# Kernel optimization log

Hardware: AMD Instinct MI355X
Metric: run time of the kernel (lower is better)

Reference implementation:

```python
import jax, jax.numpy as jnp
import numpy as np

P = 16       # patch size
HEADS = 4    # attention heads
ROPE_BASE = 10000.0


def _ln(x, g, b, eps=1e-5):
    m = x.mean(-1, keepdims=True)
    v = jnp.var(x, axis=-1, keepdims=True)
    return (x - m) / jnp.sqrt(v + eps) * g + b


def _rope(x, cos, sin):
    # x: (B, N, D); cos/sin: (N, D//2); rotate consecutive pairs
    B, N, D = x.shape
    x2 = x.reshape(B, N, D // 2, 2)
    x0, x1 = x2[..., 0], x2[..., 1]
    r0 = x0 * cos - x1 * sin
    r1 = x0 * sin + x1 * cos
    return jnp.stack([r0, r1], axis=-1).reshape(B, N, D)


def setup_inputs() -> dict:
    key = jax.random.key(0)
    L, D, Hd, Cin, S, NC = 8, 256, 1024, 3, 512, 1000
    ks = jax.random.split(key, 16)
    nrm = lambda k, shape, s=0.02: jax.random.normal(k, shape, jnp.float32) * s
    f32 = jnp.float32
    return {
        "x": jax.random.normal(ks[0], (16, Cin, S, S), f32),
        "conv_w": nrm(ks[1], (D, Cin, P, P)),
        "conv_b": jnp.zeros((D,), f32),
        "cls_tok": nrm(ks[2], (1, 1, D)),
        "ln1_g": jnp.ones((L, D), f32), "ln1_b": jnp.zeros((L, D), f32),
        "wq": nrm(ks[3], (L, D, D)), "bq": jnp.zeros((L, D), f32),
        "wk": nrm(ks[4], (L, D, D)), "bk": jnp.zeros((L, D), f32),
        "wv": nrm(ks[5], (L, D, D)), "bv": jnp.zeros((L, D), f32),
        "wo": nrm(ks[6], (L, D, D)), "bo": jnp.zeros((L, D), f32),
        "ln2_g": jnp.ones((L, D), f32), "ln2_b": jnp.zeros((L, D), f32),
        "w1": nrm(ks[7], (L, D, Hd)), "b1": jnp.zeros((L, Hd), f32),
        "w2": nrm(ks[8], (L, Hd, D)), "b2": jnp.zeros((L, D), f32),
        "lnf_g": jnp.ones((D,), f32), "lnf_b": jnp.zeros((D,), f32),
        "head_w": nrm(ks[9], (D, NC)), "head_b": jnp.zeros((NC,), f32),
    }


def reference(x, conv_w, conv_b, cls_tok, ln1_g, ln1_b, wq, bq, wk, bk, wv, bv,
              wo, bo, ln2_g, ln2_b, w1, b1, w2, b2, lnf_g, lnf_b, head_w, head_b):
    B, C, H, W = x.shape
    D = conv_w.shape[0]
    dh = D // HEADS
    # patch embed: conv with stride==kernel == blocked einsum
    xp = x.reshape(B, C, H // P, P, W // P, P)
    patches = jnp.einsum('bchpwq,dcpq->bhwd', xp, conv_w).reshape(B, -1, D) + conv_b
    tok = jnp.concatenate([jnp.broadcast_to(cls_tok, (B, 1, D)), patches], axis=1)
    N = tok.shape[1]  # n_patches + 1
    # rope tables over full d_model (applied pre head-split, as pos_module(q,k,pos))
    pos = jnp.arange(N, dtype=jnp.float32)
    inv_freq = 1.0 / (ROPE_BASE ** (jnp.arange(0, D, 2, dtype=jnp.float32) / D))
    ang = pos[:, None] * inv_freq                    # (N, D/2)
    cos, sin = jnp.cos(ang), jnp.sin(ang)
    scale = 1.0 / np.sqrt(dh).astype(np.float32)

    def block(h, p):
        l1g, l1b, Wq, Bq, Wk, Bk, Wv, Bv, Wo, Bo, l2g, l2b, W1, B1, W2, B2 = p
        y = _ln(h, l1g, l1b)
        q = _rope(y @ Wq + Bq, cos, sin)
        k = _rope(y @ Wk + Bk, cos, sin)
        v = y @ Wv + Bv
        qh = q.reshape(B, N, HEADS, dh)
        kh = k.reshape(B, N, HEADS, dh)
        vh = v.reshape(B, N, HEADS, dh)
        sc = jnp.einsum('bqhd,bkhd->bhqk', qh, kh) * scale
        a = jax.nn.softmax(sc, axis=-1)
        ctx = jnp.einsum('bhqk,bkhd->bqhd', a, vh).reshape(B, N, D)
        h = h + (ctx @ Wo + Bo)
        y2 = _ln(h, l2g, l2b)
        h = h + jax.nn.gelu(y2 @ W1 + B1, approximate=False) @ W2 + B2
        return h, None

    params = (ln1_g, ln1_b, wq, bq, wk, bk, wv, bv, wo, bo, ln2_g, ln2_b, w1, b1, w2, b2)
    out, _ = jax.lax.scan(block, tok, params)
    out = _ln(out, lnf_g, lnf_b)
    return out[:, 0] @ head_w + head_b
```

## Files before the change

### kernel.cpp

```cpp
#include <hip/hip_runtime.h>
#include <hip/hip_bf16.h>
#include <math.h>

#define BATCH 16
#define CIN 3
#define SIMG 512
#define PPATCH 16
#define DMODEL 256
#define HIDDEN 1024
#define LAYERS 8
#define NHEADS 4
#define DHEAD 64
#define NTOK 1025
#define NROWS (BATCH * NTOK)
#define NCLS 1000
#define VSTR 1032

typedef __attribute__((ext_vector_type(8))) short bf16x8;
typedef __attribute__((ext_vector_type(4))) float f32x4;

#define MFMA16(a, b, c) __builtin_amdgcn_mfma_f32_16x16x32_bf16(a, b, c, 0, 0, 0)

__device__ __forceinline__ ushort f2bf(float f) {
    union { float f; unsigned u; } v; v.f = f;
    unsigned r = v.u + 0x7fff + ((v.u >> 16) & 1);
    return (ushort)(r >> 16);
}
__device__ __forceinline__ float bf2f(ushort u) {
    union { unsigned u; float f; } v; v.u = ((unsigned)u) << 16;
    return v.f;
}
__device__ __forceinline__ unsigned pk2(ushort a, ushort b) {
    return (unsigned)a | ((unsigned)b << 16);
}
__device__ __forceinline__ int swz16(int row, int bcol) {
    return row * 128 + (bcol ^ ((row & 7) << 4));
}
__device__ __forceinline__ void gload16(const void* g, void* l) {
    __builtin_amdgcn_global_load_lds(
        (const __attribute__((address_space(1))) unsigned int*)g,
        (__attribute__((address_space(3))) unsigned int*)l,
        16, 0, 0);
}

__global__ void rope_tab_kernel(float* __restrict__ cosb, float* __restrict__ sinb) {
    int i = blockIdx.x * 256 + threadIdx.x;
    if (i >= NTOK * 128) return;
    int n = i >> 7, j = i & 127;
    float inv = powf(10000.0f, -(float)(2 * j) / 256.0f);
    float ang = (float)n * inv;
    cosb[i] = cosf(ang);
    sinb[i] = sinf(ang);
}

__global__ void cls_kernel(const float* __restrict__ cls, float* __restrict__ tok) {
    int i = blockIdx.x * 256 + threadIdx.x;
    int b = i >> 8, d = i & 255;
    tok[(size_t)b * NTOK * DMODEL + d] = cls[d];
}

__global__ void cvt_bf16_kernel(const float* __restrict__ in, ushort* __restrict__ out, int n) {
    int base = (blockIdx.x * 256 + threadIdx.x) * 4;
    if (base >= n) return;
    float4 v = *(const float4*)(in + base);
    *(ushort4*)(out + base) = make_ushort4(f2bf(v.x), f2bf(v.y), f2bf(v.z), f2bf(v.w));
}

__global__ __launch_bounds__(256) void transpose_cvt_kernel(
    const float* __restrict__ W, ushort* __restrict__ WT, int K, int N,
    long wl, long wtl)
{
    __shared__ float t[32][33];
    int l = blockIdx.z;
    W  += (size_t)l * wl;
    WT += (size_t)l * wtl;
    int kb = blockIdx.y * 32, nb = blockIdx.x * 32;
    int tx = threadIdx.x & 31, ty = threadIdx.x >> 5;
    #pragma unroll
    for (int i = 0; i < 32; i += 8)
        t[ty + i][tx] = W[(size_t)(kb + ty + i) * N + nb + tx];
    __syncthreads();
    #pragma unroll
    for (int i = 0; i < 32; i += 8)
        WT[(size_t)(nb + ty + i) * K + kb + tx] = f2bf(t[tx][ty + i]);
}

__global__ __launch_bounds__(256) void ln_kernel(
    const float* __restrict__ in, ushort* __restrict__ outp,
    const float* __restrict__ g, const float* __restrict__ bta, int nrows)
{
    int row = blockIdx.x * 4 + (threadIdx.x >> 6);
    int lane = threadIdx.x & 63;
    if (row >= nrows) return;
    const float* xr = in + (size_t)row * DMODEL;
    float4 v = *(const float4*)(xr + lane * 4);
    float s = v.x + v.y + v.z + v.w;
    float ss = v.x * v.x + v.y * v.y + v.z * v.z + v.w * v.w;
    #pragma unroll
    for (int m = 1; m < 64; m <<= 1) {
        s += __shfl_xor(s, m, 64);
        ss += __shfl_xor(ss, m, 64);
    }
    float mean = s * (1.0f / 256.0f);
    float var = ss * (1.0f / 256.0f) - mean * mean;
    float inv = rsqrtf(var + 1e-5f);
    float4 gv = *(const float4*)(g + lane * 4);
    float4 bv = *(const float4*)(bta + lane * 4);
    ushort4 o = make_ushort4(f2bf((v.x - mean) * inv * gv.x + bv.x),
                             f2bf((v.y - mean) * inv * gv.y + bv.y),
                             f2bf((v.z - mean) * inv * gv.z + bv.z),
                             f2bf((v.w - mean) * inv * gv.w + bv.w));
    *(ushort4*)(outp + (size_t)row * DMODEL + lane * 4) = o;
}

__global__ __launch_bounds__(256) void patch_gemm(
    const float* __restrict__ x, const ushort* __restrict__ Wb,
    const float* __restrict__ bias, float* __restrict__ h)
{
    __shared__ __align__(16) ushort As[128 * 64];
    __shared__ __align__(16) ushort Bs[64 * 64];
    int bid = blockIdx.x;
    int xcd = bid & 7, idx = bid >> 3;
    int m0 = (xcd * 16 + (idx >> 2)) * 128;
    int n0 = (idx & 3) * 64;
    int tid = threadIdx.x;
    int w = tid >> 6, l = tid & 63;
    int lr = l & 15, lg = l >> 4;
    int wm = w & 1, wn = w >> 1;
    f32x4 acc[4][2] = {};

    for (int k0 = 0; k0 < 768; k0 += 64) {
        __syncthreads();
        #pragma unroll
        for (int i = 0; i < 4; ++i) {
            int id = tid + 256 * i; int r = id >> 3, c8 = id & 7;
            int m = m0 + r;
            int b_ = m >> 10, pi = m & 1023, ph = pi >> 5, pw = pi & 31;
            int k = k0 + c8 * 8;
            int c = k >> 8, rem = k & 255, pr = rem >> 4, q = rem & 15;
            const float* src = x + ((size_t)((b_ * 3 + c) * SIMG) + ph * 16 + pr) * SIMG
                                 + pw * 16 + q;
            float4 v0 = *(const float4*)src;
            float4 v1 = *(const float4*)(src + 4);
            uint4 t;
            t.x = pk2(f2bf(v0.x), f2bf(v0.y));
            t.y = pk2(f2bf(v0.z), f2bf(v0.w));
            t.z = pk2(f2bf(v1.x), f2bf(v1.y));
            t.w = pk2(f2bf(v1.z), f2bf(v1.w));
            *(uint4*)((char*)As + swz16(r, c8 * 16)) = t;
        }
        #pragma unroll
        for (int i = 0; i < 2; ++i) {
            int id = tid + 256 * i; int r = id >> 3, c8 = id & 7;
            uint4 t = *(const uint4*)(Wb + (size_t)(n0 + r) * 768 + k0 + c8 * 8);
            *(uint4*)((char*)Bs + swz16(r, c8 * 16)) = t;
        }
        __syncthreads();
        #pragma unroll
        for (int ks = 0; ks < 2; ++ks) {
            bf16x8 af[4];
            #pragma unroll
            for (int mf = 0; mf < 4; ++mf)
                af[mf] = *(const bf16x8*)((char*)As + swz16(wm * 64 + mf * 16 + lr, ks * 64 + lg * 16));
            #pragma unroll
            for (int nf = 0; nf < 2; ++nf) {
                bf16x8 bfr = *(const bf16x8*)((char*)Bs + swz16(wn * 32 + nf * 16 + lr, ks * 64 + lg * 16));
                #pragma unroll
                for (int mf = 0; mf < 4; ++mf)
                    acc[mf][nf] = MFMA16(af[mf], bfr, acc[mf][nf]);
            }
        }
    }
    #pragma unroll
    for (int mf = 0; mf < 4; ++mf) {
        #pragma unroll
        for (int nf = 0; nf < 2; ++nf) {
            int n = n0 + wn * 32 + nf * 16 + lr;
            float bb = bias[n];
            #pragma unroll
            for (int e = 0; e < 4; ++e) {
                int m = m0 + wm * 64 + mf * 16 + lg * 4 + e;
                int b_ = m >> 10, pi = m & 1023;
                h[((size_t)(b_ * NTOK + 1 + pi)) * DMODEL + n] = acc[mf][nf][e] + bb;
            }
        }
    }
}

__global__ __launch_bounds__(512) void gemm_qkv(
    const ushort* __restrict__ A, const ushort* __restrict__ WT,
    const float* __restrict__ bq, const float* __restrict__ bk,
    const float* __restrict__ bv,
    ushort* __restrict__ qbf, ushort* __restrict__ kbf, ushort* __restrict__ vT,
    const float* __restrict__ cosb, const float* __restrict__ sinb, int M)
{
    __shared__ __align__(16) ushort As[128 * 64];
    __shared__ __align__(16) ushort Bs[128 * 64];
    int bid = blockIdx.x;
    int xcd = bid & 7, idx = bid >> 3;
    int mt = xcd * 17 + idx / 6;
    int m0 = mt * 128;
    if (m0 >= M) return;
    int n0 = (idx % 6) * 128;
    int tid = threadIdx.x;
    int w = tid >> 6, l = tid & 63;
    int lr = l & 15, lg = l >> 4;
    int wm = w & 1, wn = w >> 1;
    int wb0 = (tid & ~63) * 16;
    f32x4 acc[4][2] = {};

    for (int k0 = 0; k0 < 256; k0 += 64) {
        __syncthreads();
        #pragma unroll
        for (int i = 0; i < 2; ++i) {
            int id = tid + 512 * i; int r = id >> 3, c8 = id & 7;
            int mrow = m0 + r; if (mrow > M - 1) mrow = M - 1;
            int c8s = c8 ^ (r & 7);
            gload16(A + (size_t)mrow * 256 + k0 + c8s * 8, (char*)As + wb0 + i * 8192);
        }
        #pragma unroll
        for (int i = 0; i < 2; ++i) {
            int id = tid + 512 * i; int r = id >> 3, c8 = id & 7;
            int c8s = c8 ^ (r & 7);
            gload16(WT + (size_t)(n0 + r) * 256 + k0 + c8s * 8, (char*)Bs + wb0 + i * 8192);
        }
        __syncthreads();
        #pragma unroll
        for (int ks = 0; ks < 2; ++ks) {
            bf16x8 af[4], bf[2];
            #pragma unroll
            for (int mf = 0; mf < 4; ++mf)
                af[mf] = *(const bf16x8*)((char*)As + swz16(wm * 64 + mf * 16 + lr, ks * 64 + lg * 16));
            #pragma unroll
            for (int nf = 0; nf < 2; ++nf)
                bf[nf] = *(const bf16x8*)((char*)Bs + swz16(wn * 32 + nf * 16 + lr, ks * 64 + lg * 16));
            #pragma unroll
            for (int nf = 0; nf < 2; ++nf)
                #pragma unroll
                for (int mf = 0; mf < 4; ++mf)
                    acc[mf][nf] = MFMA16(af[mf], bf[nf], acc[mf][nf]);
        }
    }

    int sel = (n0 + wn * 32) >> 8;
    int ncb = (n0 + wn * 32) & 255;
    const float* bp = sel == 0 ? bq : (sel == 1 ? bk : bv);
    #pragma unroll
    for (int mf = 0; mf < 4; ++mf) {
        #pragma unroll
        for (int nf = 0; nf < 2; ++nf) {
            int nc = ncb + nf * 16 + lr;
            float bb = bp[nc];
            #pragma unroll
            for (int e = 0; e < 4; ++e) {
                int m = m0 + wm * 64 + mf * 16 + lg * 4 + e;
                float v = acc[mf][nf][e] + bb;
                if (sel < 2) {
                    float pv = __shfl_xor(v, 1, 64);
                    int tok = m % NTOK;
                    int j = nc >> 1;
                    float c = cosb[tok * 128 + j], s = sinb[tok * 128 + j];
                    float o = (nc & 1) ? (pv * s + v * c) : (v * c - pv * s);
                    if (m < M) {
                        ushort* dst = sel == 0 ? qbf : kbf;
                        dst[(size_t)m * DMODEL + nc] = f2bf(o);
                    }
                } else if (m < M) {
                    int b_ = m / NTOK, tok = m - b_ * NTOK;
                    vT[((size_t)(b_ * 256 + nc)) * VSTR + tok] = f2bf(v);
                }
            }
        }
    }
}

__global__ __launch_bounds__(512) void gemm_gelu(
    const ushort* __restrict__ A, const ushort* __restrict__ WT,
    const float* __restrict__ bias, ushort* __restrict__ Cbf, int M)
{
    __shared__ __align__(16) ushort As[128 * 64];
    __shared__ __align__(16) ushort Bs[128 * 64];
    int bid = blockIdx.x;
    int xcd = bid & 7, idx = bid >> 3;
    int mt = xcd * 17 + (idx >> 3);
    int m0 = mt * 128;
    if (m0 >= M) return;
    int n0 = (idx & 7) * 128;
    int tid = threadIdx.x;
    int w = tid >> 6, l = tid & 63;
    int lr = l & 15, lg = l >> 4;
    int wm = w & 1, wn = w >> 1;
    int wb0 = (tid & ~63) * 16;
    f32x4 acc[4][2] = {};

    for (int k0 = 0; k0 < 256; k0 += 64) {
        __syncthreads();
        #pragma unroll
        for (int i = 0; i < 2; ++i) {
            int id = tid + 512 * i; int r = id >> 3, c8 = id & 7;
            int mrow = m0 + r; if (mrow > M - 1) mrow = M - 1;
            int c8s = c8 ^ (r & 7);
            gload16(A + (size_t)mrow * 256 + k0 + c8s * 8, (char*)As + wb0 + i * 8192);
        }
        #pragma unroll
        for (int i = 0; i < 2; ++i) {
            int id = tid + 512 * i; int r = id >> 3, c8 = id & 7;
            int c8s = c8 ^ (r & 7);
            gload16(WT + (size_t)(n0 + r) * 256 + k0 + c8s * 8, (char*)Bs + wb0 + i * 8192);
        }
        __syncthreads();
        #pragma unroll
        for (int ks = 0; ks < 2; ++ks) {
            bf16x8 af[4], bf[2];
            #pragma unroll
            for (int mf = 0; mf < 4; ++mf)
                af[mf] = *(const bf16x8*)((char*)As + swz16(wm * 64 + mf * 16 + lr, ks * 64 + lg * 16));
            #pragma unroll
            for (int nf = 0; nf < 2; ++nf)
                bf[nf] = *(const bf16x8*)((char*)Bs + swz16(wn * 32 + nf * 16 + lr, ks * 64 + lg * 16));
            #pragma unroll
            for (int nf = 0; nf < 2; ++nf)
                #pragma unroll
                for (int mf = 0; mf < 4; ++mf)
                    acc[mf][nf] = MFMA16(af[mf], bf[nf], acc[mf][nf]);
        }
    }

    #pragma unroll
    for (int mf = 0; mf < 4; ++mf) {
        #pragma unroll
        for (int nf = 0; nf < 2; ++nf) {
            int n = n0 + wn * 32 + nf * 16 + lr;
            float bb = bias[n];
            #pragma unroll
            for (int e = 0; e < 4; ++e) {
                int m = m0 + wm * 64 + mf * 16 + lg * 4 + e;
                float v = acc[mf][nf][e] + bb;
                if (m < M) {
                    float gg = 0.5f * v * (1.0f + erff(v * 0.70710678118f));
                    Cbf[(size_t)m * HIDDEN + n] = f2bf(gg);
                }
            }
        }
    }
}

__global__ __launch_bounds__(512) void gemm_res_ln(
    const ushort* __restrict__ A, const ushort* __restrict__ WT,
    const float* __restrict__ bias, float* __restrict__ hres,
    ushort* __restrict__ ybf, const float* __restrict__ g,
    const float* __restrict__ beta, int M, int K)
{
    __shared__ __align__(16) ushort As[64 * 64];
    __shared__ __align__(16) ushort Bs[256 * 64];
    __shared__ float psum[8][64], psq[8][64];
    __shared__ float mv[64][2];
    int tid = threadIdx.x;
    int w = tid >> 6, l = tid & 63;
    int lr = l & 15, lg = l >> 4;
    int m0 = blockIdx.x * 64;
    int wb0 = (tid & ~63) * 16;
    f32x4 acc[4][2] = {};

    for (int k0 = 0; k0 < K; k0 += 64) {
        __syncthreads();
        {
            int r = tid >> 3, c8 = tid & 7;
            int mrow = m0 + r; if (mrow > M - 1) mrow = M - 1;
            int c8s = c8 ^ (r & 7);
            gload16(A + (size_t)mrow * K + k0 + c8s * 8, (char*)As + wb0);
        }
        #pragma unroll
        for (int i = 0; i < 4; ++i) {
            int id = tid + 512 * i; int r = id >> 3, c8 = id & 7;
            int c8s = c8 ^ (r & 7);
            gload16(WT + (size_t)r * K + k0 + c8s * 8, (char*)Bs + wb0 + i * 8192);
        }
        __syncthreads();
        #pragma unroll
        for (int ks = 0; ks < 2; ++ks) {
            bf16x8 af[4], bf[2];
            #pragma unroll
            for (int mf = 0; mf < 4; ++mf)
                af[mf] = *(const bf16x8*)((char*)As + swz16(mf * 16 + lr, ks * 64 + lg * 16));
            #pragma unroll
            for (int nf = 0; nf < 2; ++nf)
                bf[nf] = *(const bf16x8*)((char*)Bs + swz16(w * 32 + nf * 16 + lr, ks * 64 + lg * 16));
            #pragma unroll
            for (int nf = 0; nf < 2; ++nf)
                #pragma unroll
                for (int mf = 0; mf < 4; ++mf)
                    acc[mf][nf] = MFMA16(af[mf], bf[nf], acc[mf][nf]);
        }
    }

    #pragma unroll
    for (int mf = 0; mf < 4; ++mf) {
        #pragma unroll
        for (int nf = 0; nf < 2; ++nf) {
            int n = w * 32 + nf * 16 + lr;
            float bb = bias[n];
            #pragma unroll
            for (int e = 0; e < 4; ++e) {
                int m = m0 + mf * 16 + lg * 4 + e;
                float hv = acc[mf][nf][e] + bb;
                if (m < M) hv += hres[(size_t)m * DMODEL + n];
                acc[mf][nf][e] = hv;
            }
        }
    }
    #pragma unroll
    for (int mf = 0; mf < 4; ++mf) {
        #pragma unroll
        for (int e = 0; e < 4; ++e) {
            float s = acc[mf][0][e] + acc[mf][1][e];
            float q = acc[mf][0][e] * acc[mf][0][e] + acc[mf][1][e] * acc[mf][1][e];
            #pragma unroll
            for (int t = 1; t < 16; t <<= 1) {
                s += __shfl_xor(s, t, 16);
                q += __shfl_xor(q, t, 16);
            }
            if (lr == 0) {
                int r64 = mf * 16 + lg * 4 + e;
                psum[w][r64] = s;
                psq[w][r64] = q;
            }
        }
    }
    __syncthreads();
    if (tid < 64) {
        float s = 0.f, q = 0.f;
        #pragma unroll
        for (int ww = 0; ww < 8; ++ww) { s += psum[ww][tid]; q += psq[ww][tid]; }
        float mean = s * (1.0f / 256.0f);
        float var = q * (1.0f / 256.0f) - mean * mean;
        mv[tid][0] = mean;
        mv[tid][1] = rsqrtf(var + 1e-5f);
    }
    __syncthreads();
    #pragma unroll
    for (int mf = 0; mf < 4; ++mf) {
        #pragma unroll
        for (int e = 0; e < 4; ++e) {
            int r64 = mf * 16 + lg * 4 + e;
            int m = m0 + r64;
            if (m >= M) continue;
            float mean = mv[r64][0], rstd = mv[r64][1];
            #pragma unroll
            for (int nf = 0; nf < 2; ++nf) {
                int n = w * 32 + nf * 16 + lr;
                float hv = acc[mf][nf][e];
                hres[(size_t)m * DMODEL + n] = hv;
                ybf[(size_t)m * DMODEL + n] = f2bf((hv - mean) * rstd * g[n] + beta[n]);
            }
        }
    }
}

__global__ __launch_bounds__(256) void flash_mfma(
    const ushort* __restrict__ Qb, const ushort* __restrict__ Kb,
    const ushort* __restrict__ Vt, ushort* __restrict__ Ctx)
{
    __shared__ __align__(16) ushort QPs[64 * 64];
    __shared__ __align__(16) ushort Ks[64 * 64];
    __shared__ __align__(16) ushort Vs[64 * 64];

    int bid = blockIdx.x;
    int xcd = bid & 7, idx = bid >> 3;
    int bh = xcd * 8 + idx / 17;
    int q0 = (idx % 17) * 64;
    int tid = threadIdx.x;
    int w = tid >> 6, l = tid & 63;
    int lr = l & 15, lg = l >> 4;
    int b = bh >> 2, h = bh & 3;
    const size_t rowbase = (size_t)b * NTOK;
    const size_t vbase = (size_t)(b * 256 + h * 64) * VSTR;
    int wb0 = (tid & ~63) * 16;

    int id0 = tid, id1 = tid + 256;
    int r0 = id0 >> 3, c80 = id0 & 7;
    int r1 = id1 >> 3, c81 = id1 & 7;
    int d0 = swz16(r0, c80 * 16), d1 = swz16(r1, c81 * 16);

    {
        int qr0 = q0 + r0; if (qr0 > 1024) qr0 = 1024;
        int qr1 = q0 + r1; if (qr1 > 1024) qr1 = 1024;
        int c80s = c80 ^ (r0 & 7), c81s = c81 ^ (r1 & 7);
        gload16(Qb + (rowbase + qr0) * 256 + h * 64 + c80s * 8, (char*)QPs + wb0);
        gload16(Qb + (rowbase + qr1) * 256 + h * 64 + c81s * 8, (char*)QPs + wb0 + 4096);
    }

    uint4 kreg0, kreg1, vreg0, vreg1;
    auto loadKV = [&](int kt) {
        int kr0 = kt * 64 + r0; if (kr0 > 1024) kr0 = 1024;
        int kr1 = kt * 64 + r1; if (kr1 > 1024) kr1 = 1024;
        kreg0 = *(const uint4*)(Kb + (rowbase + kr0) * 256 + h * 64 + c80 * 8);
        kreg1 = *(const uint4*)(Kb + (rowbase + kr1) * 256 + h * 64 + c81 * 8);
        vreg0 = *(const uint4*)(Vt + vbase + (size_t)r0 * VSTR + kt * 64 + c80 * 8);
        vreg1 = *(const uint4*)(Vt + vbase + (size_t)r1 * VSTR + kt * 64 + c81 * 8);
    };
    auto writeKV = [&]() {
        *(uint4*)((char*)Ks + d0) = kreg0;
        *(uint4*)((char*)Ks + d1) = kreg1;
        *(uint4*)((char*)Vs + d0) = vreg0;
        *(uint4*)((char*)Vs + d1) = vreg1;
    };

    loadKV(0);
    __syncthreads();
    writeKV();
    __syncthreads();

    bf16x8 qreg[2];
    #pragma unroll
    for (int ks = 0; ks < 2; ++ks)
        qreg[ks] = *(const bf16x8*)((char*)QPs + swz16(w * 16 + lr, ks * 64 + lg * 16));

    f32x4 po[4] = {};
    float lsum = 0.f;

    for (int kt = 0; kt < 17; ++kt) {
        if (kt < 16) loadKV(kt + 1);

        f32x4 sa[4] = {};
        #pragma unroll
        for (int ks = 0; ks < 2; ++ks) {
            #pragma unroll
            for (int nf = 0; nf < 4; ++nf) {
                bf16x8 kb = *(const bf16x8*)((char*)Ks + swz16(nf * 16 + lr, ks * 64 + lg * 16));
                sa[nf] = MFMA16(kb, qreg[ks], sa[nf]);
            }
        }

        #pragma unroll
        for (int nf = 0; nf < 4; ++nf) {
            float p0, p1, p2, p3;
            {
                int kc0 = kt * 64 + nf * 16 + lg * 4;
                p0 = (kc0 + 0 > 1024) ? 0.f : __expf(sa[nf][0] * 0.125f);
                p1 = (kc0 + 1 > 1024) ? 0.f : __expf(sa[nf][1] * 0.125f);
                p2 = (kc0 + 2 > 1024) ? 0.f : __expf(sa[nf][2] * 0.125f);
                p3 = (kc0 + 3 > 1024) ? 0.f : __expf(sa[nf][3] * 0.125f);
            }
            lsum += (p0 + p1) + (p2 + p3);
            uint2 t;
            t.x = pk2(f2bf(p0), f2bf(p1));
            t.y = pk2(f2bf(p2), f2bf(p3));
            *(uint2*)((char*)QPs + swz16(w * 16 + lr, nf * 32 + lg * 8)) = t;
        }

        #pragma unroll
        for (int ks = 0; ks < 2; ++ks) {
            bf16x8 pa = *(const bf16x8*)((char*)QPs + swz16(w * 16 + lr, ks * 64 + lg * 16));
            #pragma unroll
            for (int d = 0; d < 4; ++d) {
                bf16x8 vb = *(const bf16x8*)((char*)Vs + swz16(d * 16 + lr, ks * 64 + lg * 16));
                po[d] = MFMA16(pa, vb, po[d]);
            }
        }

        __syncthreads();
        if (kt < 16) writeKV();
        __syncthreads();
    }

    lsum += __shfl_xor(lsum, 16, 64);
    lsum += __shfl_xor(lsum, 32, 64);
    #pragma unroll
    for (int e = 0; e < 4; ++e) {
        float le = __shfl(lsum, lg * 4 + e, 16);
        int qr = q0 + w * 16 + lg * 4 + e;
        if (qr <= 1024) {
            float inv = 1.0f / le;
            #pragma unroll
            for (int d = 0; d < 4; ++d)
                Ctx[(rowbase + qr) * 256 + h * 64 + d * 16 + lr] = f2bf(po[d][e] * inv);
        }
    }
}

__global__ void head_kernel(const ushort* __restrict__ ybf,
                            const float* __restrict__ hw,
                            const float* __restrict__ hb,
                            float* __restrict__ out)
{
    int i = blockIdx.x * 256 + threadIdx.x;
    if (i >= BATCH * NCLS) return;
    int b = i / NCLS, c = i % NCLS;
    const ushort* xr = ybf + (size_t)b * NTOK * DMODEL;
    float acc = hb[c];
    for (int t = 0; t < DMODEL; ++t) acc += bf2f(xr[t]) * hw[t * NCLS + c];
    out[i] = acc;
}

extern "C" void kernel_launch(void* const* d_in, const int* in_sizes, int n_in,
                              void* d_out, int out_size, void* d_ws, size_t ws_size,
                              hipStream_t stream) {
    const float* x      = (const float*)d_in[0];
    const float* conv_w = (const float*)d_in[1];
    const float* conv_b = (const float*)d_in[2];
    const float* cls_tok= (const float*)d_in[3];
    const float* ln1_g  = (const float*)d_in[4];
    const float* ln1_b  = (const float*)d_in[5];
    const float* wq     = (const float*)d_in[6];
    const float* bq     = (const float*)d_in[7];
    const float* wk     = (const float*)d_in[8];
    const float* bk     = (const float*)d_in[9];
    const float* wv     = (const float*)d_in[10];
    const float* bv     = (const float*)d_in[11];
    const float* wo     = (const float*)d_in[12];
    const float* bo     = (const float*)d_in[13];
    const float* ln2_g  = (const float*)d_in[14];
    const float* ln2_b  = (const float*)d_in[15];
    const float* w1     = (const float*)d_in[16];
    const float* b1     = (const float*)d_in[17];
    const float* w2     = (const float*)d_in[18];
    const float* b2     = (const float*)d_in[19];
    const float* lnf_g  = (const float*)d_in[20];
    const float* lnf_b  = (const float*)d_in[21];
    const float* head_w = (const float*)d_in[22];
    const float* head_b = (const float*)d_in[23];

    char* p = (char*)d_ws;
    float* h    = (float*)p;            p += (size_t)NROWS * DMODEL * 4;
    float* cosb = (float*)p;            p += (size_t)NTOK * 128 * 4;
    float* sinb = (float*)p;            p += (size_t)NTOK * 128 * 4;
    ushort* ybf = (ushort*)p;           p += (size_t)NROWS * DMODEL * 2;
    ushort* cbf = (ushort*)p;           p += (size_t)NROWS * DMODEL * 2;
    ushort* qbf = (ushort*)p;           p += (size_t)NROWS * DMODEL * 2;
    ushort* kbf = (ushort*)p;           p += (size_t)NROWS * DMODEL * 2;
    ushort* vT  = (ushort*)p;           p += (size_t)BATCH * 256 * VSTR * 2 + 256;
    ushort* hidbf = (ushort*)p;         p += (size_t)NROWS * HIDDEN * 2;
    ushort* wqkvT = (ushort*)p;         p += (size_t)LAYERS * 768 * DMODEL * 2;
    ushort* woT = (ushort*)p;           p += (size_t)LAYERS * DMODEL * DMODEL * 2;
    ushort* w1T = (ushort*)p;           p += (size_t)LAYERS * DMODEL * HIDDEN * 2;
    ushort* w2T = (ushort*)p;           p += (size_t)LAYERS * DMODEL * HIDDEN * 2;
    ushort* cwb = (ushort*)p;           p += (size_t)DMODEL * 768 * 2;

    transpose_cvt_kernel<<<dim3(8, 8, LAYERS), 256, 0, stream>>>(
        wq, wqkvT, 256, 256, 65536, 196608);
    transpose_cvt_kernel<<<dim3(8, 8, LAYERS), 256, 0, stream>>>(
        wk, wqkvT + 65536, 256, 256, 65536, 196608);
    transpose_cvt_kernel<<<dim3(8, 8, LAYERS), 256, 0, stream>>>(
        wv, wqkvT + 131072, 256, 256, 65536, 196608);
    transpose_cvt_kernel<<<dim3(8, 8, LAYERS), 256, 0, stream>>>(
        wo, woT, 256, 256, 65536, 65536);
    transpose_cvt_kernel<<<dim3(32, 8, LAYERS), 256, 0, stream>>>(
        w1, w1T, 256, 1024, 262144, 262144);
    transpose_cvt_kernel<<<dim3(8, 32, LAYERS), 256, 0, stream>>>(
        w2, w2T, 1024, 256, 262144, 262144);
    rope_tab_kernel<<<(NTOK * 128 + 255) / 256, 256, 0, stream>>>(cosb, sinb);
    cls_kernel<<<BATCH, 256, 0, stream>>>(cls_tok, h);
    cvt_bf16_kernel<<<192, 256, 0, stream>>>(conv_w, cwb, DMODEL * 768);
    patch_gemm<<<512, 256, 0, stream>>>(x, cwb, conv_b, h);

    const int M = NROWS;
    int grln = (M + 63) / 64;

    ln_kernel<<<(M + 3) / 4, 256, 0, stream>>>(h, ybf, ln1_g, ln1_b, M);

    for (int l = 0; l < LAYERS; ++l) {
        const ushort* WqkvT = wqkvT + (size_t)l * 768 * DMODEL;
        const ushort* WoT = woT + (size_t)l * DMODEL * DMODEL;
        const ushort* W1T = w1T + (size_t)l * DMODEL * HIDDEN;
        const ushort* W2T = w2T + (size_t)l * DMODEL * HIDDEN;

        gemm_qkv<<<816, 512, 0, stream>>>(ybf, WqkvT, bq + l * DMODEL, bk + l * DMODEL,
                                          bv + l * DMODEL, qbf, kbf, vT, cosb, sinb, M);
        flash_mfma<<<1088, 256, 0, stream>>>(qbf, kbf, vT, cbf);
        gemm_res_ln<<<grln, 512, 0, stream>>>(cbf, WoT, bo + l * DMODEL, h, ybf,
                                              ln2_g + l * DMODEL, ln2_b + l * DMODEL,
                                              M, DMODEL);
        gemm_gelu<<<1088, 512, 0, stream>>>(ybf, W1T, b1 + l * HIDDEN, hidbf, M);
        const float* ng = (l < LAYERS - 1) ? ln1_g + (l + 1) * DMODEL : lnf_g;
        const float* nb = (l < LAYERS - 1) ? ln1_b + (l + 1) * DMODEL : lnf_b;
        gemm_res_ln<<<grln, 512, 0, stream>>>(hidbf, W2T, b2 + l * DMODEL, h, ybf,
                                              ng, nb, M, HIDDEN);
    }
    head_kernel<<<(BATCH * NCLS + 255) / 256, 256, 0, stream>>>(ybf, head_w, head_b,
                                                                (float*)d_out);
}
```

Baseline: 1.234 ms.

## Process two 64-row query subtiles per flash-attention block to reuse K/V tiles

Each attention block now covers 128 queries as two 64-row subtiles. Both subtiles share each staged K/V tile, which halves K/V global loads per query and halves the grid size. Q fragments are loaded straight from global memory into registers instead of going through shared memory, and one startup barrier is dropped. In exchange, the last query tile (a single valid row) now wastes a full 128-row tile of compute, register use per thread rises, and the smaller grid may balance less well across CUs.

Result: slower. 1.309 ms (+6.0%).

```diff
diff --git a/kernel.cpp b/kernel.cpp
--- a/kernel.cpp
+++ b/kernel.cpp
@@ -461,33 +461,33 @@
     const ushort* __restrict__ Qb, const ushort* __restrict__ Kb,
     const ushort* __restrict__ Vt, ushort* __restrict__ Ctx)
 {
-    __shared__ __align__(16) ushort QPs[64 * 64];
+    __shared__ __align__(16) ushort Ps[64 * 64];
     __shared__ __align__(16) ushort Ks[64 * 64];
     __shared__ __align__(16) ushort Vs[64 * 64];
 
     int bid = blockIdx.x;
     int xcd = bid & 7, idx = bid >> 3;
-    int bh = xcd * 8 + idx / 17;
-    int q0 = (idx % 17) * 64;
+    int bh = xcd * 8 + idx / 9;
+    int q0 = (idx % 9) * 128;
     int tid = threadIdx.x;
     int w = tid >> 6, l = tid & 63;
     int lr = l & 15, lg = l >> 4;
     int b = bh >> 2, h = bh & 3;
     const size_t rowbase = (size_t)b * NTOK;
     const size_t vbase = (size_t)(b * 256 + h * 64) * VSTR;
-    int wb0 = (tid & ~63) * 16;
 
     int id0 = tid, id1 = tid + 256;
     int r0 = id0 >> 3, c80 = id0 & 7;
     int r1 = id1 >> 3, c81 = id1 & 7;
     int d0 = swz16(r0, c80 * 16), d1 = swz16(r1, c81 * 16);
 
-    {
-        int qr0 = q0 + r0; if (qr0 > 1024) qr0 = 1024;
-        int qr1 = q0 + r1; if (qr1 > 1024) qr1 = 1024;
-        int c80s = c80 ^ (r0 & 7), c81s = c81 ^ (r1 & 7);
-        gload16(Qb + (rowbase + qr0) * 256 + h * 64 + c80s * 8, (char*)QPs + wb0);
-        gload16(Qb + (rowbase + qr1) * 256 + h * 64 + c81s * 8, (char*)QPs + wb0 + 4096);
+    bf16x8 qreg[2][2];
+    #pragma unroll
+    for (int qs = 0; qs < 2; ++qs) {
+        int qr = q0 + qs * 64 + w * 16 + lr; if (qr > 1024) qr = 1024;
+        const ushort* qrow = Qb + (rowbase + qr) * 256 + h * 64 + lg * 8;
+        qreg[qs][0] = *(const bf16x8*)(qrow);
+        qreg[qs][1] = *(const bf16x8*)(qrow + 32);
     }
 
     uint4 kreg0, kreg1, vreg0, vreg1;
@@ -507,55 +507,52 @@
     };
 
     loadKV(0);
-    __syncthreads();
     writeKV();
     __syncthreads();
 
-    bf16x8 qreg[2];
-    #pragma unroll
-    for (int ks = 0; ks < 2; ++ks)
-        qreg[ks] = *(const bf16x8*)((char*)QPs + swz16(w * 16 + lr, ks * 64 + lg * 16));
-
-    f32x4 po[4] = {};
-    float lsum = 0.f;
+    f32x4 po[2][4] = {};
+    float lsum[2] = {0.f, 0.f};
 
     for (int kt = 0; kt < 17; ++kt) {
         if (kt < 16) loadKV(kt + 1);
 
-        f32x4 sa[4] = {};
-        #pragma unroll
-        for (int ks = 0; ks < 2; ++ks) {
+        #pragma unroll
+        for (int qs = 0; qs < 2; ++qs) {
+            f32x4 sa[4] = {};
+            #pragma unroll
+            for (int ks = 0; ks < 2; ++ks) {
+                #pragma unroll
+                for (int nf = 0; nf < 4; ++nf) {
+                    bf16x8 kb = *(const bf16x8*)((char*)Ks + swz16(nf * 16 + lr, ks * 64 + lg * 16));
+                    sa[nf] = MFMA16(kb, qreg[qs][ks], sa[nf]);
+                }
+            }
+
             #pragma unroll
             for (int nf = 0; nf < 4; ++nf) {
-                bf16x8 kb = *(const bf16x8*)((char*)Ks + swz16(nf * 16 + lr, ks * 64 + lg * 16));
-                sa[nf] = MFMA16(kb, qreg[ks], sa[nf]);
-            }
-        }
-
-        #pragma unroll
-        for (int nf = 0; nf < 4; ++nf) {
-            float p0, p1, p2, p3;
-            {
-                int kc0 = kt * 64 + nf * 16 + lg * 4;
-                p0 = (kc0 + 0 > 1024) ? 0.f : __expf(sa[nf][0] * 0.125f);
-                p1 = (kc0 + 1 > 1024) ? 0.f : __expf(sa[nf][1] * 0.125f);
-                p2 = (kc0 + 2 > 1024) ? 0.f : __expf(sa[nf][2] * 0.125f);
-                p3 = (kc0 + 3 > 1024) ? 0.f : __expf(sa[nf][3] * 0.125f);
-            }
-            lsum += (p0 + p1) + (p2 + p3);
-            uint2 t;
-            t.x = pk2(f2bf(p0), f2bf(p1));
-            t.y = pk2(f2bf(p2), f2bf(p3));
-            *(uint2*)((char*)QPs + swz16(w * 16 + lr, nf * 32 + lg * 8)) = t;
-        }
-
-        #pragma unroll
-        for (int ks = 0; ks < 2; ++ks) {
-            bf16x8 pa = *(const bf16x8*)((char*)QPs + swz16(w * 16 + lr, ks * 64 + lg * 16));
-            #pragma unroll
-            for (int d = 0; d < 4; ++d) {
-                bf16x8 vb = *(const bf16x8*)((char*)Vs + swz16(d * 16 + lr, ks * 64 + lg * 16));
-                po[d] = MFMA16(pa, vb, po[d]);
+                float p0, p1, p2, p3;
+                {
+                    int kc0 = kt * 64 + nf * 16 + lg * 4;
+                    p0 = (kc0 + 0 > 1024) ? 0.f : __expf(sa[nf][0] * 0.125f);
+                    p1 = (kc0 + 1 > 1024) ? 0.f : __expf(sa[nf][1] * 0.125f);
+                    p2 = (kc0 + 2 > 1024) ? 0.f : __expf(sa[nf][2] * 0.125f);
+                    p3 = (kc0 + 3 > 1024) ? 0.f : __expf(sa[nf][3] * 0.125f);
+                }
+                lsum[qs] += (p0 + p1) + (p2 + p3);
+                uint2 t;
+                t.x = pk2(f2bf(p0), f2bf(p1));
+                t.y = pk2(f2bf(p2), f2bf(p3));
+                *(uint2*)((char*)Ps + swz16(w * 16 + lr, nf * 32 + lg * 8)) = t;
+            }
+
+            #pragma unroll
+            for (int ks = 0; ks < 2; ++ks) {
+                bf16x8 pa = *(const bf16x8*)((char*)Ps + swz16(w * 16 + lr, ks * 64 + lg * 16));
+                #pragma unroll
+                for (int d = 0; d < 4; ++d) {
+                    bf16x8 vb = *(const bf16x8*)((char*)Vs + swz16(d * 16 + lr, ks * 64 + lg * 16));
+                    po[qs][d] = MFMA16(pa, vb, po[qs][d]);
+                }
             }
         }
 
@@ -564,17 +561,21 @@
         __syncthreads();
     }
 
-    lsum += __shfl_xor(lsum, 16, 64);
-    lsum += __shfl_xor(lsum, 32, 64);
-    #pragma unroll
-    for (int e = 0; e < 4; ++e) {
-        float le = __shfl(lsum, lg * 4 + e, 16);
-        int qr = q0 + w * 16 + lg * 4 + e;
-        if (qr <= 1024) {
-            float inv = 1.0f / le;
-            #pragma unroll
-            for (int d = 0; d < 4; ++d)
-                Ctx[(rowbase + qr) * 256 + h * 64 + d * 16 + lr] = f2bf(po[d][e] * inv);
+    #pragma unroll
+    for (int qs = 0; qs < 2; ++qs) {
+        float ls = lsum[qs];
+        ls += __shfl_xor(ls, 16, 64);
+        ls += __shfl_xor(ls, 32, 64);
+        #pragma unroll
+        for (int e = 0; e < 4; ++e) {
+            float le = __shfl(ls, lg * 4 + e, 16);
+            int qr = q0 + qs * 64 + w * 16 + lg * 4 + e;
+            if (qr <= 1024) {
+                float inv = 1.0f / le;
+                #pragma unroll
+                for (int d = 0; d < 4; ++d)
+                    Ctx[(rowbase + qr) * 256 + h * 64 + d * 16 + lr] = f2bf(po[qs][d][e] * inv);
+            }
         }
     }
 }
@@ -667,7 +668,7 @@
 
         gemm_qkv<<<816, 512, 0, stream>>>(ybf, WqkvT, bq + l * DMODEL, bk + l * DMODEL,
                                           bv + l * DMODEL, qbf, kbf, vT, cosb, sinb, M);
-        flash_mfma<<<1088, 256, 0, stream>>>(qbf, kbf, vT, cbf);
+        flash_mfma<<<576, 256, 0, stream>>>(qbf, kbf, vT, cbf);
         gemm_res_ln<<<grln, 512, 0, stream>>>(cbf, WoT, bo + l * DMODEL, h, ybf,
                                               ln2_g + l * DMODEL, ln2_b + l * DMODEL,
                                               M, DMODEL);
```
